# Optimization experiments

Hardware: AMD Instinct MI355X
Metric: run time of the kernel (lower is better)

## Reference

```python
import jax, jax.numpy as jnp
import numpy as np

T = 0.2
EPS = 1e-05


def setup_inputs() -> dict:
    key = jax.random.key(0)
    k1, k2 = jax.random.split(key)
    N, D, NUM_CLASSES = 8192, 128, 128
    inp = jax.random.normal(k1, (N, D), dtype=jnp.float32)
    label = jax.random.randint(k2, (N,), 0, NUM_CLASSES, dtype=jnp.int64)
    return {"input": inp, "label": label}


def reference(input, label):
    # Pairwise cosine similarity: dot(x_i, x_j) / max(||x_i|| * ||x_j||, eps)
    norms = jnp.sqrt(jnp.sum(input * input, axis=1))            # [N]
    denom = jnp.maximum(norms[:, None] * norms[None, :], EPS)   # [N, N]
    sim = (input @ input.T) / denom                             # [N, N]

    mask = (label[:, None] == label[None, :]).astype(input.dtype)  # same-label mask
    e = jnp.exp(sim / T)
    e = e - jnp.diag(jnp.diag(e))                               # zero the diagonal

    pos = mask * e                                              # positives (diag already 0)
    unsim = jnp.sum(e - pos, axis=-1, keepdims=True)            # [N, 1] negatives row-sum
    ratio = pos / (pos + unsim)                                 # per-pair NT-Xent prob
    safe = jnp.where(ratio > 0, ratio, 1.0)                     # loss[loss<=0] = 1
    loss_sum = jnp.sum(-jnp.log(safe))

    # number of off-diagonal positive pairs
    off_diag_mask = mask - jnp.diag(jnp.diag(mask))
    n_pos = jnp.count_nonzero(off_diag_mask).astype(input.dtype)
    return loss_sum / n_pos
```

## Files before the change

### kernel.cpp

```cpp
#include <hip/hip_runtime.h>
#include <math.h>

typedef float f32x4 __attribute__((ext_vector_type(4)));
typedef __attribute__((address_space(3))) unsigned int lds_u32;
typedef __attribute__((address_space(1))) const unsigned int glb_u32;


__global__ __launch_bounds__(256) void norm_kernel(
    const float* __restrict__ X, unsigned char* __restrict__ Y8,
    float* __restrict__ out, float scaleAB) {
  int t = threadIdx.x;
  int row = blockIdx.x * 8 + (t >> 5);
  int l32 = t & 31;
  float4 v = ((const float4*)(X + (size_t)row * 128))[l32];
  float s = v.x * v.x + v.y * v.y + v.z * v.z + v.w * v.w;
  s += __shfl_xor(s, 1);
  s += __shfl_xor(s, 2);
  s += __shfl_xor(s, 4);
  s += __shfl_xor(s, 8);
  s += __shfl_xor(s, 16);
  float inv = scaleAB * rsqrtf(fmaxf(s, 1e-24f));
  int pk = __builtin_amdgcn_cvt_pk_fp8_f32(v.x * inv, v.y * inv, 0, false);
  pk = __builtin_amdgcn_cvt_pk_fp8_f32(v.z * inv, v.w * inv, pk, true);
  int chunk = l32 >> 2;
  int off = ((chunk ^ (row & 7)) << 4) + ((l32 & 3) << 2);
  *(unsigned int*)(Y8 + (size_t)row * 128 + off) = (unsigned)pk;
  if (blockIdx.x == 0 && t == 0) out[0] = 0.f;
}

__global__ __launch_bounds__(256, 4) void pass1_kernel(
    const unsigned char* __restrict__ Y8, const int* __restrict__ lab,
    float* __restrict__ P, float* __restrict__ Q, float* __restrict__ S,
    int N) {
  __shared__ unsigned char Bs[3][64][128];
  __shared__ int labC[512];
  __shared__ float sS[4];

  const int b = blockIdx.x;
  const int bi = b >> 4, c = b & 15;
  const int i0 = bi * 128;
  const int j0 = c * 512;
  const int t = threadIdx.x;
  const int w = t >> 6, lane = t & 63;
  const int quad = lane >> 4, l16 = lane & 15;
  const int rbase = w * 32;
  const int sw = l16 & 7;

  labC[t] = lab[j0 + t];
  labC[t + 256] = lab[j0 + 256 + t];

  long af[4][2];
#pragma unroll
  for (int ks = 0; ks < 4; ++ks) {
    const int ch = ks * 2 + (quad >> 1);
    const int off = ((ch ^ sw) << 4) + ((quad & 1) << 3);
#pragma unroll
    for (int p = 0; p < 2; ++p)
      af[ks][p] =
          *(const long*)(Y8 + (size_t)(i0 + rbase + p * 16 + l16) * 128 + off);
  }
  int lr[2][4];
#pragma unroll
  for (int pi = 0; pi < 2; ++pi)
#pragma unroll
    for (int r = 0; r < 4; ++r)
      lr[pi][r] = lab[i0 + rbase + pi * 16 + quad * 4 + r];

  __syncthreads();

#pragma unroll
  for (int pt = 0; pt < 3; ++pt) {
    const unsigned char* src = Y8 + (size_t)(j0 + pt * 64) * 128;
    unsigned char* dst = (unsigned char*)&Bs[pt][0][0];
#pragma unroll
    for (int k = 0; k < 2; ++k) {
      const int c0 = w * 64 + k * 256;
      const int cc = c0 + lane;
      __builtin_amdgcn_global_load_lds((glb_u32*)(src + (size_t)cc * 16),
                                       (lds_u32*)(dst + c0 * 16), 16, 0, 0);
    }
  }

  float trow[2][4] = {};
  float pr[2][4] = {};
  float sacc = 0.f;

#pragma unroll
  for (int jt = 0; jt < 8; ++jt) {
    const int buf = jt % 3;
    const int jt0 = j0 + jt * 64;
    const int rem = 7 - jt;

    if (rem >= 2)
      asm volatile("s_waitcnt vmcnt(4)" ::: "memory");
    else if (rem == 1)
      asm volatile("s_waitcnt vmcnt(2)" ::: "memory");
    else
      asm volatile("s_waitcnt vmcnt(0)" ::: "memory");
    asm volatile("s_barrier" ::: "memory");
    __builtin_amdgcn_sched_barrier(0);

    int lc[4];
#pragma unroll
    for (int pj = 0; pj < 4; ++pj) lc[pj] = labC[jt * 64 + pj * 16 + l16];

    f32x4 acc[2][4] = {};
#pragma unroll
    for (int ks = 0; ks < 4; ++ks) {
      const int ch = ks * 2 + (quad >> 1);
      const int off = ((ch ^ sw) << 4) + ((quad & 1) << 3);
      long bf[4];
#pragma unroll
      for (int p = 0; p < 4; ++p)
        bf[p] = *(const long*)&Bs[buf][p * 16 + l16][off];
#pragma unroll
      for (int pi = 0; pi < 2; ++pi)
#pragma unroll
        for (int pj = 0; pj < 4; ++pj)
          acc[pi][pj] = __builtin_amdgcn_mfma_f32_16x16x32_fp8_fp8(
              af[ks][pi], bf[pj], acc[pi][pj], 0, 0, 0);
    }

    const bool dphase = ((jt0 >> 7) == bi);
    if (dphase) {
#pragma unroll
      for (int pi = 0; pi < 2; ++pi)
#pragma unroll
        for (int pj = 0; pj < 4; ++pj)
#pragma unroll
          for (int r = 0; r < 4; ++r) {
            const float s2 = acc[pi][pj][r];
            const float e = exp2f(s2);
            const int rowl = rbase + pi * 16 + quad * 4 + r;
            const bool self = (i0 + rowl) == (jt0 + pj * 16 + l16);
            const bool match = (lr[pi][r] == lc[pj]) && !self;
            trow[pi][r] += self ? 0.f : e;
            pr[pi][r] += match ? e : 0.f;
            sacc += match ? s2 : 0.f;
          }
    } else {
#pragma unroll
      for (int pi = 0; pi < 2; ++pi)
#pragma unroll
        for (int pj = 0; pj < 4; ++pj)
#pragma unroll
          for (int r = 0; r < 4; ++r) {
            const float s2 = acc[pi][pj][r];
            const float e = exp2f(s2);
            const bool match = (lr[pi][r] == lc[pj]);
            trow[pi][r] += e;
            pr[pi][r] += match ? e : 0.f;
            sacc += match ? s2 : 0.f;
          }
    }

    __builtin_amdgcn_sched_barrier(0);
    asm volatile("s_barrier" ::: "memory");
    __builtin_amdgcn_sched_barrier(0);

    if (jt < 5) {
      const unsigned char* src = Y8 + (size_t)(jt0 + 192) * 128;
      unsigned char* dst = (unsigned char*)&Bs[buf][0][0];
#pragma unroll
      for (int k = 0; k < 2; ++k) {
        const int c0 = w * 64 + k * 256;
        const int cc = c0 + lane;
        __builtin_amdgcn_global_load_lds((glb_u32*)(src + (size_t)cc * 16),
                                         (lds_u32*)(dst + c0 * 16), 16, 0, 0);
      }
    }
  }

#pragma unroll
  for (int pi = 0; pi < 2; ++pi)
#pragma unroll
    for (int r = 0; r < 4; ++r) {
      float v = trow[pi][r], q = pr[pi][r];
      v += __shfl_xor(v, 1);
      q += __shfl_xor(q, 1);
      v += __shfl_xor(v, 2);
      q += __shfl_xor(q, 2);
      v += __shfl_xor(v, 4);
      q += __shfl_xor(q, 4);
      v += __shfl_xor(v, 8);
      q += __shfl_xor(q, 8);
      if (l16 == 0) {
        const int row = rbase + pi * 16 + quad * 4 + r;
        P[c * N + i0 + row] = v;
        Q[c * N + i0 + row] = q;
      }
    }
#pragma unroll
  for (int m = 1; m < 64; m <<= 1) sacc += __shfl_xor(sacc, m);
  if (lane == 0) sS[w] = sacc;
  __syncthreads();
  if (t == 0)
    S[b] = (sS[0] + sS[1] + sS[2] + sS[3]) * 0.69314718056f;
}

__global__ __launch_bounds__(256) void finalize_kernel(
    const int* __restrict__ lab, const float* __restrict__ P,
    const float* __restrict__ Q, const float* __restrict__ S,
    float* __restrict__ out, int N) {
  __shared__ int hist[256];
  __shared__ float red[4];
  const int b = blockIdx.x, t = threadIdx.x;
  const int lane = t & 63, w = t >> 6;
  hist[t] = 0;
  __syncthreads();
  for (int i = t; i < N; i += 256) atomicAdd(&hist[lab[i] & 255], 1);
  __syncthreads();

  const int i = b * 256 + t;
  float tot = 0.f, p = 0.f;
#pragma unroll
  for (int cc = 0; cc < 16; ++cc) {
    tot += P[cc * N + i];
    p += Q[cc * N + i];
  }
  const float u = tot - p;
  const float cnti = (float)(hist[lab[i] & 255] - 1);
  float local = cnti * __logf(u) + p / u;
  if (t < 32) local -= S[b * 32 + t];
#pragma unroll
  for (int m = 1; m < 64; m <<= 1) local += __shfl_xor(local, m);
  if (lane == 0) red[w] = local;
  __syncthreads();
  if (t == 0) {
    float np = 0.f;
    for (int k = 0; k < 256; ++k) {
      const float m = (float)hist[k];
      np += m * m;
    }
    atomicAdd(out, (red[0] + red[1] + red[2] + red[3]) / (np - (float)N));
  }
}

extern "C" void kernel_launch(void* const* d_in, const int* in_sizes, int n_in,
                              void* d_out, int out_size, void* d_ws,
                              size_t ws_size, hipStream_t stream) {
  const float* X = (const float*)d_in[0];
  const int* lab = (const int*)d_in[1];
  float* out = (float*)d_out;

  const int N = in_sizes[1];

  unsigned char* Y8 = (unsigned char*)d_ws;
  float* P = (float*)(Y8 + (size_t)N * 128);
  float* Q = P + 16 * (size_t)N;
  float* S = Q + 16 * (size_t)N;

  const float scaleAB = 2.68579102f;

  norm_kernel<<<N / 8, 256, 0, stream>>>(X, Y8, out, scaleAB);

  const int nblk = (N / 128) * 16;
  pass1_kernel<<<nblk, 256, 0, stream>>>(Y8, lab, P, Q, S, N);
  finalize_kernel<<<32, 256, 0, stream>>>(lab, P, Q, S, out, N);
}
```

Baseline: 98.59 us.

## Switch B-tile prefetch from triple to double buffering with block barriers

Replaces the three-stage LDS ring, which used explicit vmcnt waits and raw s_barrier, with a two-buffer scheme. Each iteration issues the next tile's global-to-LDS copy at its top and ends with __syncthreads. The main loop is no longer unrolled. This cuts LDS use and code size, but shortens the prefetch distance and makes every iteration wait for the outstanding load at the barrier. It also loses the compile-time specialization of the diagonal-tile branch per iteration.

Result: slower. 102.0 us (+3.4%).

```diff
diff --git a/kernel.cpp b/kernel.cpp
--- a/kernel.cpp
+++ b/kernel.cpp
@@ -32,7 +32,7 @@
     const unsigned char* __restrict__ Y8, const int* __restrict__ lab,
     float* __restrict__ P, float* __restrict__ Q, float* __restrict__ S,
     int N) {
-  __shared__ unsigned char Bs[3][64][128];
+  __shared__ unsigned char Bs[2][64][128];
   __shared__ int labC[512];
   __shared__ float sS[4];
 
@@ -46,6 +46,14 @@
   const int rbase = w * 32;
   const int sw = l16 & 7;
 
+#pragma unroll
+  for (int k = 0; k < 2; ++k) {
+    const int c0 = w * 64 + k * 256;
+    const int cc = c0 + lane;
+    __builtin_amdgcn_global_load_lds(
+        (glb_u32*)(Y8 + (size_t)j0 * 128 + (size_t)cc * 16),
+        (lds_u32*)((unsigned char*)&Bs[0][0][0] + c0 * 16), 16, 0, 0);
+  }
   labC[t] = lab[j0 + t];
   labC[t + 256] = lab[j0 + 256 + t];
 
@@ -66,39 +74,28 @@
     for (int r = 0; r < 4; ++r)
       lr[pi][r] = lab[i0 + rbase + pi * 16 + quad * 4 + r];
 
-  __syncthreads();
-
-#pragma unroll
-  for (int pt = 0; pt < 3; ++pt) {
-    const unsigned char* src = Y8 + (size_t)(j0 + pt * 64) * 128;
-    unsigned char* dst = (unsigned char*)&Bs[pt][0][0];
-#pragma unroll
-    for (int k = 0; k < 2; ++k) {
-      const int c0 = w * 64 + k * 256;
-      const int cc = c0 + lane;
-      __builtin_amdgcn_global_load_lds((glb_u32*)(src + (size_t)cc * 16),
-                                       (lds_u32*)(dst + c0 * 16), 16, 0, 0);
-    }
-  }
-
   float trow[2][4] = {};
   float pr[2][4] = {};
   float sacc = 0.f;
 
-#pragma unroll
+  __syncthreads();
+
+#pragma unroll 1
   for (int jt = 0; jt < 8; ++jt) {
-    const int buf = jt % 3;
+    const int cur = jt & 1;
     const int jt0 = j0 + jt * 64;
-    const int rem = 7 - jt;
-
-    if (rem >= 2)
-      asm volatile("s_waitcnt vmcnt(4)" ::: "memory");
-    else if (rem == 1)
-      asm volatile("s_waitcnt vmcnt(2)" ::: "memory");
-    else
-      asm volatile("s_waitcnt vmcnt(0)" ::: "memory");
-    asm volatile("s_barrier" ::: "memory");
-    __builtin_amdgcn_sched_barrier(0);
+
+    if (jt < 7) {
+      const unsigned char* src = Y8 + (size_t)(jt0 + 64) * 128;
+      unsigned char* dst = (unsigned char*)&Bs[cur ^ 1][0][0];
+#pragma unroll
+      for (int k = 0; k < 2; ++k) {
+        const int c0 = w * 64 + k * 256;
+        const int cc = c0 + lane;
+        __builtin_amdgcn_global_load_lds((glb_u32*)(src + (size_t)cc * 16),
+                                         (lds_u32*)(dst + c0 * 16), 16, 0, 0);
+      }
+    }
 
     int lc[4];
 #pragma unroll
@@ -112,7 +109,7 @@
       long bf[4];
 #pragma unroll
       for (int p = 0; p < 4; ++p)
-        bf[p] = *(const long*)&Bs[buf][p * 16 + l16][off];
+        bf[p] = *(const long*)&Bs[cur][p * 16 + l16][off];
 #pragma unroll
       for (int pi = 0; pi < 2; ++pi)
 #pragma unroll
@@ -153,22 +150,7 @@
             sacc += match ? s2 : 0.f;
           }
     }
-
-    __builtin_amdgcn_sched_barrier(0);
-    asm volatile("s_barrier" ::: "memory");
-    __builtin_amdgcn_sched_barrier(0);
-
-    if (jt < 5) {
-      const unsigned char* src = Y8 + (size_t)(jt0 + 192) * 128;
-      unsigned char* dst = (unsigned char*)&Bs[buf][0][0];
-#pragma unroll
-      for (int k = 0; k < 2; ++k) {
-        const int c0 = w * 64 + k * 256;
-        const int cc = c0 + lane;
-        __builtin_amdgcn_global_load_lds((glb_u32*)(src + (size_t)cc * 16),
-                                         (lds_u32*)(dst + c0 * 16), 16, 0, 0);
-      }
-    }
+    __syncthreads();
   }
 
 #pragma unroll
```
